# Optimization experiments

Measured on AMD Instinct MI355X. Metric: run time of the kernel, lower is better.

Reference implementation:

```python
import jax, jax.numpy as jnp
import numpy as np

N_NODES = 100000
N_EDGES = 1600000
D_IN = 128
D_OUT = 128
N_GRAPHS = 256


def setup_inputs() -> dict:
    key = jax.random.key(0)
    k1, k2, k3, k4 = jax.random.split(key, 4)
    H = jax.random.normal(k1, (N_NODES, D_IN), dtype=jnp.float32)
    edge_index = jax.random.randint(k2, (2, N_EDGES), 0, N_NODES, dtype=jnp.int64)
    batch = jnp.sort(jax.random.randint(k3, (N_NODES,), 0, N_GRAPHS, dtype=jnp.int64))
    # Kaiming-normal init: std = sqrt(2 / fan_in)
    W = jax.random.normal(k4, (D_IN, D_OUT), dtype=jnp.float32) * np.float32(np.sqrt(2.0 / D_IN))
    return {"H": H, "edge_index": edge_index, "batch": batch, "W": W}


def reference(H, edge_index, batch, W):
    N = H.shape[0]
    src, dst = edge_index[0], edge_index[1]
    # message passing: gather source features, scatter_add into destinations
    agg = jax.ops.segment_sum(H[src], dst, num_segments=N)  # [N, D]
    out = H + agg
    # virtual node: per-graph mean, broadcast back to nodes
    sums = jax.ops.segment_sum(out, batch, num_segments=N_GRAPHS)            # [G, D]
    counts = jax.ops.segment_sum(jnp.ones((N, 1), out.dtype), batch,
                                 num_segments=N_GRAPHS)                       # [G, 1]
    vmean = sums / jnp.maximum(counts, 1.0)
    out = out + vmean[batch]
    # dense transform + activation
    return jax.nn.relu(out @ W)
```

## Files before the change

### kernel.cpp

```cpp
#include <hip/hip_runtime.h>

#define DIM 128
#define NGRAPH 256

#define CHUNK 512
#define CHB 9
#define MAXNB 256
#define EPB 4096
#define EPT (EPB / 256)
#define FCAP 14336

typedef __attribute__((ext_vector_type(8))) short short8;
typedef __attribute__((ext_vector_type(4))) float f32x4;

__device__ inline unsigned int bpack2(float lo, float hi) {
  unsigned int ul = __float_as_uint(lo);
  unsigned int uh = __float_as_uint(hi);
  ul = (ul + 0x7fffu + ((ul >> 16) & 1u)) >> 16;
  uh = (uh + 0x7fffu + ((uh >> 16) & 1u)) & 0xffff0000u;
  return ul | uh;
}

__device__ inline float4 bunpack4(uint2 v) {
  float4 r;
  r.x = __uint_as_float(v.x << 16);
  r.y = __uint_as_float(v.x & 0xffff0000u);
  r.z = __uint_as_float(v.y << 16);
  r.w = __uint_as_float(v.y & 0xffff0000u);
  return r;
}

__global__ __launch_bounds__(256) void k_prep(const float4* __restrict__ H4,
    uint2* __restrict__ Hb, int n4,
    const int* __restrict__ dst, unsigned short* __restrict__ bh, int E,
    int NBLK) {
  __shared__ unsigned int hist[MAXNB];
  int blk = blockIdx.x, t = threadIdx.x;
  int i = blk * 256 + t;
  if (i < n4) {
    float4 a = H4[i];
    uint2 r;
    r.x = bpack2(a.x, a.y);
    r.y = bpack2(a.z, a.w);
    Hb[i] = r;
  }
  if (blk < NBLK) {
    hist[t] = 0;
    __syncthreads();
    int base = blk * EPB;
#pragma unroll
    for (int k = 0; k < EPT; ++k) {
      int e = base + k * 256 + t;
      if (e < E) atomicAdd(&hist[((unsigned)dst[e]) >> CHB], 1);
    }
    __syncthreads();
    bh[(size_t)blk * MAXNB + t] = (unsigned short)hist[t];
  }
}

__global__ __launch_bounds__(256) void k_bhist(const int* __restrict__ dst,
    unsigned short* __restrict__ bh, int E) {
  __shared__ unsigned int hist[MAXNB];
  int blk = blockIdx.x, t = threadIdx.x;
  hist[t] = 0;
  __syncthreads();
  int base = blk * EPB;
#pragma unroll
  for (int i = 0; i < EPT; ++i) {
    int e = base + i * 256 + t;
    if (e < E) atomicAdd(&hist[((unsigned)dst[e]) >> CHB], 1);
  }
  __syncthreads();
  bh[(size_t)blk * MAXNB + t] = (unsigned short)hist[t];
}

__global__ __launch_bounds__(256) void k_bscan(unsigned short* __restrict__ bh,
    unsigned int* __restrict__ btot, int NBLK) {
  __shared__ unsigned int tmp[256];
  int b = blockIdx.x, t = threadIdx.x;
  int i0 = 2 * t, i1 = 2 * t + 1;
  unsigned int a0 = (i0 < NBLK) ? bh[(size_t)i0 * MAXNB + b] : 0u;
  unsigned int a1 = (i1 < NBLK) ? bh[(size_t)i1 * MAXNB + b] : 0u;
  unsigned int ps = a0 + a1;
  tmp[t] = ps;
  __syncthreads();
  for (int off = 1; off < 256; off <<= 1) {
    unsigned int x = (t >= off) ? tmp[t - off] : 0u;
    __syncthreads();
    tmp[t] += x;
    __syncthreads();
  }
  unsigned int ex = tmp[t] - ps;
  if (i0 < NBLK) bh[(size_t)i0 * MAXNB + b] = (unsigned short)ex;
  if (i1 < NBLK) bh[(size_t)i1 * MAXNB + b] = (unsigned short)(ex + a0);
  if (t == 255) btot[b] = tmp[255];
}

__global__ __launch_bounds__(256) void k_bscan2(const unsigned int* __restrict__ btot,
    unsigned int* __restrict__ bbase, int* __restrict__ offs, int N, int E) {
  __shared__ unsigned int s[256];
  int t = threadIdx.x;
  unsigned int v = btot[t];
  s[t] = v;
  __syncthreads();
  for (int off = 1; off < 256; off <<= 1) {
    unsigned int x = (t >= off) ? s[t - off] : 0u;
    __syncthreads();
    s[t] += x;
    __syncthreads();
  }
  bbase[t] = s[t] - v;
  if (t == 255) { bbase[256] = s[255]; offs[N] = E; }
}

__global__ __launch_bounds__(256) void k_part(const int* __restrict__ src,
    const int* __restrict__ dst, const unsigned short* __restrict__ bh,
    const unsigned int* __restrict__ bbase, unsigned int* __restrict__ pack, int E) {
  __shared__ unsigned int hist[MAXNB];
  __shared__ unsigned int sc[MAXNB];
  __shared__ unsigned int gbase[MAXNB];
  __shared__ unsigned int lpack[EPB];
  __shared__ unsigned short lbkt[EPB];
  __shared__ unsigned int totS;
  int blk = blockIdx.x, t = threadIdx.x;
  hist[t] = 0;
  __syncthreads();

  int base = blk * EPB;
  unsigned int pk[EPT];
  int bk[EPT];
  unsigned int rk[EPT];
#pragma unroll
  for (int i = 0; i < EPT; ++i) {
    int e = base + i * 256 + t;
    if (e < E) {
      unsigned int s = (unsigned)src[e], d = (unsigned)dst[e];
      pk[i] = (s << CHB) | (d & (CHUNK - 1));
      int b = (int)(d >> CHB);
      bk[i] = b;
      rk[i] = atomicAdd(&hist[b], 1u);
    } else {
      bk[i] = -1;
    }
  }
  __syncthreads();

  unsigned int c = hist[t];
  sc[t] = c;
  __syncthreads();
  for (int off = 1; off < 256; off <<= 1) {
    unsigned int x = (t >= off) ? sc[t - off] : 0u;
    __syncthreads();
    sc[t] += x;
    __syncthreads();
  }
  if (t == 255) totS = sc[255];
  hist[t] = sc[t] - c;
  gbase[t] = bbase[t] + (unsigned int)bh[(size_t)blk * MAXNB + t];
  __syncthreads();

#pragma unroll
  for (int i = 0; i < EPT; ++i) {
    if (bk[i] >= 0) {
      unsigned int slot = hist[bk[i]] + rk[i];
      lpack[slot] = pk[i];
      lbkt[slot] = (unsigned short)bk[i];
    }
  }
  __syncthreads();

  unsigned int tot = totS;
  for (unsigned int s = t; s < tot; s += 256) {
    int b = lbkt[s];
    unsigned int local = s - hist[b];
    pack[gbase[b] + local] = lpack[s];
  }
}

__global__ __launch_bounds__(256) void k_fine(unsigned int* __restrict__ pack,
    const unsigned int* __restrict__ bbase, int* __restrict__ offs, int N) {
  __shared__ unsigned int lp[FCAP];
  __shared__ unsigned int cnt[CHUNK];
  __shared__ unsigned int cur[CHUNK];
  __shared__ unsigned int tmp[256];
  int b = blockIdx.x, t = threadIdx.x;
  unsigned int lo = bbase[b], hi = bbase[b + 1];
  int n = (int)(hi - lo);
  if (n > FCAP) n = FCAP;
  cnt[2 * t] = 0; cnt[2 * t + 1] = 0;
  __syncthreads();
  for (int i = t; i < n; i += 256) {
    unsigned int p = pack[lo + i];
    lp[i] = p;
    atomicAdd(&cnt[p & (CHUNK - 1)], 1u);
  }
  __syncthreads();
  unsigned int c0 = cnt[2 * t], c1 = cnt[2 * t + 1];
  unsigned int ps = c0 + c1;
  tmp[t] = ps;
  __syncthreads();
  for (int off = 1; off < 256; off <<= 1) {
    unsigned int x = (t >= off) ? tmp[t - off] : 0u;
    __syncthreads();
    tmp[t] += x;
    __syncthreads();
  }
  unsigned int ex = tmp[t] - ps;
  cur[2 * t] = ex;
  cur[2 * t + 1] = ex + c0;
  __syncthreads();
  int nb0 = b * CHUNK;
#pragma unroll
  for (int j = t; j < CHUNK; j += 256) {
    int node = nb0 + j;
    if (node < N) offs[node] = (int)(lo + cur[j]);
  }
  __syncthreads();
  for (int i = t; i < n; i += 256) {
    unsigned int p = lp[i];
    unsigned int r = atomicAdd(&cur[p & (CHUNK - 1)], 1u);
    pack[lo + r] = p;
  }
}

__device__ inline void bacc(uint2 v, float4& a) {
  a.x += __uint_as_float(v.x << 16);
  a.y += __uint_as_float(v.x & 0xffff0000u);
  a.z += __uint_as_float(v.y << 16);
  a.w += __uint_as_float(v.y & 0xffff0000u);
}

__global__ __launch_bounds__(256) void k_gatherbx(const uint2* __restrict__ Hb,
    const int* __restrict__ offs, const unsigned int* __restrict__ pack,
    uint2* __restrict__ Hx, int n) {
  int gid = blockIdx.x * 256 + threadIdx.x;
  int node = gid >> 6;
  if (node >= n) return;
  int lane = threadIdx.x & 63;
  int half = lane >> 5, q = lane & 31;
  float4 A = {0,0,0,0}, B = {0,0,0,0}, C = {0,0,0,0}, D = {0,0,0,0};
  int beg = offs[node], end = offs[node + 1];
  int j = beg + half;
  for (; j + 6 < end; j += 8) {
    uint2 v0 = Hb[(size_t)(pack[j + 0] >> CHB) * 32 + q];
    uint2 v1 = Hb[(size_t)(pack[j + 2] >> CHB) * 32 + q];
    uint2 v2 = Hb[(size_t)(pack[j + 4] >> CHB) * 32 + q];
    uint2 v3 = Hb[(size_t)(pack[j + 6] >> CHB) * 32 + q];
    bacc(v0, A); bacc(v1, B); bacc(v2, C); bacc(v3, D);
  }
  for (; j < end; j += 2) bacc(Hb[(size_t)(pack[j] >> CHB) * 32 + q], A);
  A.x += B.x + (C.x + D.x);
  A.y += B.y + (C.y + D.y);
  A.z += B.z + (C.z + D.z);
  A.w += B.w + (C.w + D.w);
  A.x += __shfl_xor(A.x, 32);
  A.y += __shfl_xor(A.y, 32);
  A.z += __shfl_xor(A.z, 32);
  A.w += __shfl_xor(A.w, 32);
  if (half == 0) {
    float4 b4 = bunpack4(Hb[(size_t)node * 32 + q]);
    uint2 o;
    o.x = bpack2(b4.x + A.x, b4.y + A.y);
    o.y = bpack2(b4.z + A.z, b4.w + A.w);
    Hx[(size_t)node * 32 + q] = o;
  }
}

__global__ __launch_bounds__(256) void k_gatherb(const float* __restrict__ H,
    const uint2* __restrict__ Hb, const int* __restrict__ offs,
    const unsigned int* __restrict__ pack, float* __restrict__ out, int n) {
  int gid = blockIdx.x * 256 + threadIdx.x;
  int node = gid >> 6;
  if (node >= n) return;
  int lane = threadIdx.x & 63;
  int half = lane >> 5, q = lane & 31;
  float4 A = {0,0,0,0}, B = {0,0,0,0}, C = {0,0,0,0}, D = {0,0,0,0};
  int beg = offs[node], end = offs[node + 1];
  int j = beg + half;
  for (; j + 6 < end; j += 8) {
    uint2 v0 = Hb[(size_t)(pack[j + 0] >> CHB) * 32 + q];
    uint2 v1 = Hb[(size_t)(pack[j + 2] >> CHB) * 32 + q];
    uint2 v2 = Hb[(size_t)(pack[j + 4] >> CHB) * 32 + q];
    uint2 v3 = Hb[(size_t)(pack[j + 6] >> CHB) * 32 + q];
    bacc(v0, A); bacc(v1, B); bacc(v2, C); bacc(v3, D);
  }
  for (; j < end; j += 2) bacc(Hb[(size_t)(pack[j] >> CHB) * 32 + q], A);
  A.x += B.x + (C.x + D.x);
  A.y += B.y + (C.y + D.y);
  A.z += B.z + (C.z + D.z);
  A.w += B.w + (C.w + D.w);
  A.x += __shfl_xor(A.x, 32);
  A.y += __shfl_xor(A.y, 32);
  A.z += __shfl_xor(A.z, 32);
  A.w += __shfl_xor(A.w, 32);
  if (half == 0) {
    float4 b4 = ((const float4*)H)[(size_t)node * 32 + q];
    float4 r;
    r.x = b4.x + A.x; r.y = b4.y + A.y; r.z = b4.z + A.z; r.w = b4.w + A.w;
    ((float4*)out)[(size_t)node * 32 + q] = r;
  }
}

__global__ __launch_bounds__(256) void k_gather(const float* __restrict__ H,
    const int* __restrict__ offs, const unsigned int* __restrict__ pack,
    float* __restrict__ out, int n) {
  int gid = blockIdx.x * 256 + threadIdx.x;
  int node = gid >> 6;
  if (node >= n) return;
  int lane = threadIdx.x & 63;
  const float2* H2 = (const float2*)H;
  float2 base = H2[(size_t)node * 64 + lane];
  float2 s0 = {0.f, 0.f}, s1 = {0.f, 0.f};
  int beg = offs[node], end = offs[node + 1];
  int j = beg;
  for (; j + 2 <= end; j += 2) {
    float2 v0 = H2[(size_t)(pack[j + 0] >> CHB) * 64 + lane];
    float2 v1 = H2[(size_t)(pack[j + 1] >> CHB) * 64 + lane];
    s0.x += v0.x; s0.y += v0.y;
    s1.x += v1.x; s1.y += v1.y;
  }
  for (; j < end; ++j) {
    float2 v = H2[(size_t)(pack[j] >> CHB) * 64 + lane];
    s0.x += v.x; s0.y += v.y;
  }
  float2 r;
  r.x = base.x + s0.x + s1.x;
  r.y = base.y + s0.y + s1.y;
  ((float2*)out)[(size_t)node * 64 + lane] = r;
}

__global__ __launch_bounds__(256) void k_init(const float4* __restrict__ s,
                                              float4* __restrict__ d, int n4) {
  int i = blockIdx.x * 256 + threadIdx.x;
  if (i < n4) d[i] = s[i];
}

__global__ __launch_bounds__(256) void k_scatter(const float* __restrict__ H,
    const int* __restrict__ src, const int* __restrict__ dst,
    float* __restrict__ out, int nE) {
  long long idx = (long long)blockIdx.x * 256 + threadIdx.x;
  int e = (int)(idx >> 5);
  if (e >= nE) return;
  int q = (int)(idx & 31);
  int s = src[e];
  int t = dst[e];
  const float4 h = *(const float4*)(H + (size_t)s * DIM + q * 4);
  float* o = out + (size_t)t * DIM + q * 4;
  unsafeAtomicAdd(o + 0, h.x);
  unsafeAtomicAdd(o + 1, h.y);
  unsafeAtomicAdd(o + 2, h.z);
  unsafeAtomicAdd(o + 3, h.w);
}

__global__ __launch_bounds__(256) void k_vmean4x(const uint2* __restrict__ hx,
    const int* __restrict__ batch, float* __restrict__ vmean, int n) {
  int g = blockIdx.x >> 2, c = blockIdx.x & 3;
  int lo = 0, hi = n;
  while (lo < hi) { int m = (lo + hi) >> 1; if (batch[m] < g) lo = m + 1; else hi = m; }
  int start = lo;
  hi = n;
  while (lo < hi) { int m = (lo + hi) >> 1; if (batch[m] < g + 1) lo = m + 1; else hi = m; }
  int end = lo;

  int t = threadIdx.x, rg = t >> 3, s = t & 7;
  int d4 = c * 8 + s;
  float4 acc = {0,0,0,0};
  for (int r = start + rg; r < end; r += 32) {
    float4 v = bunpack4(hx[(size_t)r * 32 + d4]);
    acc.x += v.x; acc.y += v.y; acc.z += v.z; acc.w += v.w;
  }
  __shared__ float4 sd[256];
  sd[t] = acc;
  __syncthreads();
  for (int off = 16; off >= 1; off >>= 1) {
    if (rg < off) {
      float4 o = sd[t + off * 8];
      acc.x += o.x; acc.y += o.y; acc.z += o.z; acc.w += o.w;
      sd[t] = acc;
    }
    __syncthreads();
  }
  if (rg == 0) {
    float cnt = fmaxf((float)(end - start), 1.0f);
    float4 r;
    r.x = acc.x / cnt; r.y = acc.y / cnt; r.z = acc.z / cnt; r.w = acc.w / cnt;
    ((float4*)vmean)[g * 32 + d4] = r;
  }
}

__global__ __launch_bounds__(256) void k_vmean4(const float* __restrict__ x,
    const int* __restrict__ batch, float* __restrict__ vmean, int n) {
  int g = blockIdx.x >> 2, c = blockIdx.x & 3;
  int lo = 0, hi = n;
  while (lo < hi) { int m = (lo + hi) >> 1; if (batch[m] < g) lo = m + 1; else hi = m; }
  int start = lo;
  hi = n;
  while (lo < hi) { int m = (lo + hi) >> 1; if (batch[m] < g + 1) lo = m + 1; else hi = m; }
  int end = lo;

  int t = threadIdx.x, rg = t >> 3, s = t & 7;
  int d4 = c * 8 + s;
  const float4* x4 = (const float4*)x;
  float4 acc = {0,0,0,0};
  for (int r = start + rg; r < end; r += 32) {
    float4 v = x4[(size_t)r * 32 + d4];
    acc.x += v.x; acc.y += v.y; acc.z += v.z; acc.w += v.w;
  }
  __shared__ float4 sd[256];
  sd[t] = acc;
  __syncthreads();
  for (int off = 16; off >= 1; off >>= 1) {
    if (rg < off) {
      float4 o = sd[t + off * 8];
      acc.x += o.x; acc.y += o.y; acc.z += o.z; acc.w += o.w;
      sd[t] = acc;
    }
    __syncthreads();
  }
  if (rg == 0) {
    float cnt = fmaxf((float)(end - start), 1.0f);
    float4 r;
    r.x = acc.x / cnt; r.y = acc.y / cnt; r.z = acc.z / cnt; r.w = acc.w / cnt;
    ((float4*)vmean)[g * 32 + d4] = r;
  }
}

__global__ __launch_bounds__(256) void k_wprep(const float* __restrict__ W,
                                               uint4* __restrict__ wt) {
  int gid = blockIdx.x * 256 + threadIdx.x;
  int col = gid >> 4, chunk = gid & 15;
  float f[8];
#pragma unroll
  for (int j = 0; j < 8; ++j) f[j] = W[(chunk * 8 + j) * DIM + col];
  uint4 u;
  u.x = bpack2(f[0], f[1]);
  u.y = bpack2(f[2], f[3]);
  u.z = bpack2(f[4], f[5]);
  u.w = bpack2(f[6], f[7]);
  wt[col * 16 + (chunk ^ (col & 7))] = u;
}

__global__ __launch_bounds__(256) void k_mfmax(const uint4* __restrict__ Hx,
    float* __restrict__ io, const int* __restrict__ batch,
    const float* __restrict__ vmean, const uint4* __restrict__ wt, int n) {
  __shared__ uint4 WtL[2048];
  int tid = threadIdx.x;
#pragma unroll
  for (int j = 0; j < 8; ++j) WtL[tid + 256 * j] = wt[tid + 256 * j];
  __syncthreads();

  int wid = tid >> 6;
  int lane = tid & 63;
  int q = lane & 15, hi = lane >> 4;
  int row0 = blockIdx.x * 128 + wid * 32;

  f32x4 acc[2][8];
#pragma unroll
  for (int m = 0; m < 2; ++m)
#pragma unroll
    for (int nn = 0; nn < 8; ++nn) acc[m][nn] = (f32x4){0.f, 0.f, 0.f, 0.f};

  bool okm[2];
  const uint4* xrow[2];
  const float4* vrow[2];
#pragma unroll
  for (int m = 0; m < 2; ++m) {
    int row = row0 + m * 16 + q;
    bool ok = row < n;
    okm[m] = ok;
    int g = ok ? batch[row] : 0;
    xrow[m] = Hx + (size_t)row * 16;
    vrow[m] = (const float4*)vmean + (size_t)g * 32;
  }

  for (int kk = 0; kk < 4; ++kk) {
    short8 Bf[8];
#pragma unroll
    for (int nn = 0; nn < 8; ++nn) {
      int colrow = nn * 16 + q;
      int idx = colrow * 16 + ((kk * 4 + hi) ^ (colrow & 7));
      Bf[nn] = *(short8*)&WtL[idx];
    }
    short8 Af[2];
#pragma unroll
    for (int m = 0; m < 2; ++m) {
      uint4 u = {0, 0, 0, 0};
      if (okm[m]) {
        uint4 xv = xrow[m][kk * 4 + hi];
        float4 x0 = bunpack4(*(uint2*)&xv.x);
        float4 x1 = bunpack4(*(uint2*)&xv.z);
        int c = kk * 8 + hi * 2;
        float4 v0 = vrow[m][c], v1 = vrow[m][c + 1];
        u.x = bpack2(x0.x + v0.x, x0.y + v0.y);
        u.y = bpack2(x0.z + v0.z, x0.w + v0.w);
        u.z = bpack2(x1.x + v1.x, x1.y + v1.y);
        u.w = bpack2(x1.z + v1.z, x1.w + v1.w);
      }
      Af[m] = *(short8*)&u;
    }
#pragma unroll
    for (int nn = 0; nn < 8; ++nn) {
      acc[0][nn] = __builtin_amdgcn_mfma_f32_16x16x32_bf16(Af[0], Bf[nn], acc[0][nn], 0, 0, 0);
      acc[1][nn] = __builtin_amdgcn_mfma_f32_16x16x32_bf16(Af[1], Bf[nn], acc[1][nn], 0, 0, 0);
    }
  }

#pragma unroll
  for (int m = 0; m < 2; ++m) {
    int grow0 = row0 + m * 16 + hi * 4;
#pragma unroll
    for (int nn = 0; nn < 8; ++nn) {
      int gcol = nn * 16 + q;
      f32x4 c = acc[m][nn];
#pragma unroll
      for (int r = 0; r < 4; ++r) {
        int grow = grow0 + r;
        if (grow < n) io[(size_t)grow * DIM + gcol] = fmaxf(c[r], 0.f);
      }
    }
  }
}

__global__ __launch_bounds__(256) void k_mfma(float* __restrict__ io,
    const int* __restrict__ batch, const float* __restrict__ vmean,
    const uint4* __restrict__ wt, int n) {
  __shared__ uint4 WtL[2048];
  int tid = threadIdx.x;
#pragma unroll
  for (int j = 0; j < 8; ++j) WtL[tid + 256 * j] = wt[tid + 256 * j];
  __syncthreads();

  int wid = tid >> 6;
  int lane = tid & 63;
  int q = lane & 15, hi = lane >> 4;
  int row0 = blockIdx.x * 128 + wid * 32;

  f32x4 acc[2][8];
#pragma unroll
  for (int m = 0; m < 2; ++m)
#pragma unroll
    for (int nn = 0; nn < 8; ++nn) acc[m][nn] = (f32x4){0.f, 0.f, 0.f, 0.f};

  bool okm[2];
  const float4* xrow[2];
  const float4* vrow[2];
#pragma unroll
  for (int m = 0; m < 2; ++m) {
    int row = row0 + m * 16 + q;
    bool ok = row < n;
    okm[m] = ok;
    int g = ok ? batch[row] : 0;
    xrow[m] = (const float4*)io + (size_t)row * 32;
    vrow[m] = (const float4*)vmean + (size_t)g * 32;
  }

  for (int kk = 0; kk < 4; ++kk) {
    short8 Bf[8];
#pragma unroll
    for (int nn = 0; nn < 8; ++nn) {
      int colrow = nn * 16 + q;
      int idx = colrow * 16 + ((kk * 4 + hi) ^ (colrow & 7));
      Bf[nn] = *(short8*)&WtL[idx];
    }
    short8 Af[2];
#pragma unroll
    for (int m = 0; m < 2; ++m) {
      float4 x0 = {0,0,0,0}, x1 = {0,0,0,0};
      if (okm[m]) {
        int c = kk * 8 + hi * 2;
        float4 a0 = xrow[m][c], a1 = xrow[m][c + 1];
        float4 v0 = vrow[m][c], v1 = vrow[m][c + 1];
        x0.x = a0.x + v0.x; x0.y = a0.y + v0.y; x0.z = a0.z + v0.z; x0.w = a0.w + v0.w;
        x1.x = a1.x + v1.x; x1.y = a1.y + v1.y; x1.z = a1.z + v1.z; x1.w = a1.w + v1.w;
      }
      uint4 u;
      u.x = bpack2(x0.x, x0.y);
      u.y = bpack2(x0.z, x0.w);
      u.z = bpack2(x1.x, x1.y);
      u.w = bpack2(x1.z, x1.w);
      Af[m] = *(short8*)&u;
    }
#pragma unroll
    for (int nn = 0; nn < 8; ++nn) {
      acc[0][nn] = __builtin_amdgcn_mfma_f32_16x16x32_bf16(Af[0], Bf[nn], acc[0][nn], 0, 0, 0);
      acc[1][nn] = __builtin_amdgcn_mfma_f32_16x16x32_bf16(Af[1], Bf[nn], acc[1][nn], 0, 0, 0);
    }
  }

#pragma unroll
  for (int m = 0; m < 2; ++m) {
    int grow0 = row0 + m * 16 + hi * 4;
#pragma unroll
    for (int nn = 0; nn < 8; ++nn) {
      int gcol = nn * 16 + q;
      f32x4 c = acc[m][nn];
#pragma unroll
      for (int r = 0; r < 4; ++r) {
        int grow = grow0 + r;
        if (grow < n) io[(size_t)grow * DIM + gcol] = fmaxf(c[r], 0.f);
      }
    }
  }
}

#define TRR 64
__global__ __launch_bounds__(256) void k_gemm(float* __restrict__ io,
    const int* __restrict__ batch, const float* __restrict__ vmean,
    const float* __restrict__ W, int n) {
  __shared__ float xs[TRR][DIM + 1];
  __shared__ float Wl[DIM][64];
  int tid = threadIdx.x;
  int row0 = blockIdx.x * TRR;

  for (int i = tid; i < TRR * 32; i += 256) {
    int r = i >> 5, c4 = i & 31;
    int row = row0 + r;
    float4 a;
    if (row < n) {
      int g = batch[row];
      float4 xv = *((const float4*)(io + (size_t)row * DIM) + c4);
      float4 vv = *((const float4*)(vmean + (size_t)g * DIM) + c4);
      a.x = xv.x + vv.x; a.y = xv.y + vv.y; a.z = xv.z + vv.z; a.w = xv.w + vv.w;
    } else {
      a.x = a.y = a.z = a.w = 0.f;
    }
    xs[r][c4 * 4 + 0] = a.x;
    xs[r][c4 * 4 + 1] = a.y;
    xs[r][c4 * 4 + 2] = a.z;
    xs[r][c4 * 4 + 3] = a.w;
  }

  int cg = tid & 15;
  int rg = tid >> 4;
  float acc[4][4];

  for (int jh = 0; jh < 2; ++jh) {
    __syncthreads();
    for (int i = tid; i < DIM * 16; i += 256) {
      int k = i >> 4, c4 = i & 15;
      *(float4*)&Wl[k][c4 * 4] =
          *(const float4*)(W + (size_t)k * DIM + jh * 64 + c4 * 4);
    }
    __syncthreads();

#pragma unroll
    for (int a = 0; a < 4; ++a)
#pragma unroll
      for (int b = 0; b < 4; ++b) acc[a][b] = 0.f;

    for (int k = 0; k < DIM; ++k) {
      float4 wv = *(const float4*)&Wl[k][cg * 4];
#pragma unroll
      for (int a = 0; a < 4; ++a) {
        float xv = xs[rg * 4 + a][k];
        acc[a][0] += xv * wv.x;
        acc[a][1] += xv * wv.y;
        acc[a][2] += xv * wv.z;
        acc[a][3] += xv * wv.w;
      }
    }

#pragma unroll
    for (int a = 0; a < 4; ++a) {
      int row = row0 + rg * 4 + a;
      if (row < n) {
        float4 o;
        o.x = fmaxf(acc[a][0], 0.f);
        o.y = fmaxf(acc[a][1], 0.f);
        o.z = fmaxf(acc[a][2], 0.f);
        o.w = fmaxf(acc[a][3], 0.f);
        *(float4*)(io + (size_t)row * DIM + jh * 64 + cg * 4) = o;
      }
    }
  }
}

extern "C" void kernel_launch(void* const* d_in, const int* in_sizes, int n_in,
                              void* d_out, int out_size, void* d_ws, size_t ws_size,
                              hipStream_t stream) {
  const float* H     = (const float*)d_in[0];
  const int*   ei    = (const int*)d_in[1];
  const int*   batch = (const int*)d_in[2];
  const float* W     = (const float*)d_in[3];
  float* out = (float*)d_out;

  int N = in_sizes[0] / DIM;
  int E = in_sizes[1] / 2;
  const int* src = ei;
  const int* dst = ei + E;

  int NB   = (N + CHUNK - 1) >> CHB;
  int NBLK = (E + EPB - 1) / EPB;

  size_t o = 0;
  auto carve = [&](size_t bytes) -> void* {
    void* p = (char*)d_ws + o;
    o = (o + bytes + 255) & ~(size_t)255;
    return p;
  };
  unsigned int*   pack  = (unsigned int*)carve((size_t)E * 4);
  int*            offs  = (int*)carve(((size_t)N + 1) * 4);
  unsigned short* bh    = (unsigned short*)carve((size_t)NBLK * MAXNB * 2);
  unsigned int*   btot  = (unsigned int*)carve(MAXNB * 4);
  unsigned int*   bbase = (unsigned int*)carve((MAXNB + 1) * 4);
  size_t o_csr = o;
  uint2*          Hb    = (uint2*)carve((size_t)N * DIM * 2);
  size_t o_bf = o;
  uint4*          wt    = (uint4*)carve((size_t)DIM * DIM * 2);
  size_t o_wt = o;
  uint2*          Hx    = (uint2*)carve((size_t)N * DIM * 2);
  size_t o_hx = o;
  float* vmean = (float*)bh;

  bool csr_ok = (o_csr <= ws_size) && (NB >= 1) && (NB <= MAXNB) &&
                (NBLK <= 512) && ((size_t)NBLK * MAXNB * 2 >= (size_t)NGRAPH * DIM * 4) &&
                (E / NB <= 8192);
  bool bf_ok = csr_ok && (o_bf <= ws_size);
  bool wt_ok = bf_ok && (o_wt <= ws_size) && (DIM == 128);
  bool hx_ok = wt_ok && (o_hx <= ws_size);

  if (csr_ok) {
    if (bf_ok) {
      int n4 = N * DIM / 4;
      int gprep = (n4 + 255) / 256;
      if (gprep < NBLK) gprep = NBLK;
      k_prep<<<gprep, 256, 0, stream>>>((const float4*)H, Hb, n4, dst, bh, E, NBLK);
    } else {
      k_bhist<<<NBLK, 256, 0, stream>>>(dst, bh, E);
    }
    k_bscan<<<MAXNB, 256, 0, stream>>>(bh, btot, NBLK);
    k_bscan2<<<1, 256, 0, stream>>>(btot, bbase, offs, N, E);
    k_part<<<NBLK, 256, 0, stream>>>(src, dst, bh, bbase, pack, E);
    k_fine<<<NB, 256, 0, stream>>>(pack, bbase, offs, N);
    long long gthreads = (long long)N * 64;
    int gblocks = (int)((gthreads + 255) / 256);
    if (hx_ok) {
      k_gatherbx<<<gblocks, 256, 0, stream>>>(Hb, offs, pack, Hx, N);
      k_vmean4x<<<NGRAPH * 4, 256, 0, stream>>>(Hx, batch, vmean, N);
      k_wprep<<<8, 256, 0, stream>>>(W, wt);
      k_mfmax<<<(N + 127) / 128, 256, 0, stream>>>((const uint4*)Hx, out, batch, vmean, wt, N);
      return;
    }
    if (bf_ok) {
      k_gatherb<<<gblocks, 256, 0, stream>>>(H, Hb, offs, pack, out, N);
    } else {
      k_gather<<<gblocks, 256, 0, stream>>>(H, offs, pack, out, N);
    }
  } else {
    vmean = (float*)d_ws;
    int n4 = N * DIM / 4;
    k_init<<<(n4 + 255) / 256, 256, 0, stream>>>((const float4*)H, (float4*)out, n4);
    long long sthreads = (long long)E * 32;
    k_scatter<<<(int)((sthreads + 255) / 256), 256, 0, stream>>>(H, src, dst, out, E);
  }

  k_vmean4<<<NGRAPH * 4, 256, 0, stream>>>(out, batch, vmean, N);

  if (wt_ok) {
    k_wprep<<<8, 256, 0, stream>>>(W, wt);
    k_mfma<<<(N + 127) / 128, 256, 0, stream>>>(out, batch, vmean, wt, N);
  } else {
    k_gemm<<<(N + TRR - 1) / TRR, 256, 0, stream>>>(out, batch, vmean, W, N);
  }
}
```

Before: 159.2 us.

## Widen gather to 16-byte loads, fold W prep into prep kernel, add nontemporal hints

The gather kernel now has each lane load 16 bytes (8 bf16 values), with four 16-lane groups per wavefront each taking every fourth edge, and the group results are reduced with two shuffle stages. The W bf16 packing moves into k_prep, which removes one kernel launch. Nontemporal loads and stores are added on H, pack, Hx and the final output to limit cache pollution. The wider loads halve the number of gather requests, at the cost of more accumulator registers and an extra shuffle reduction stage.

Result: slower. 170.3 us (+7.0%).

```diff
diff --git a/kernel.cpp b/kernel.cpp
--- a/kernel.cpp
+++ b/kernel.cpp
@@ -12,6 +12,7 @@
 
 typedef __attribute__((ext_vector_type(8))) short short8;
 typedef __attribute__((ext_vector_type(4))) float f32x4;
+typedef __attribute__((ext_vector_type(4))) unsigned int u32x4;
 
 __device__ inline unsigned int bpack2(float lo, float hi) {
   unsigned int ul = __float_as_uint(lo);
@@ -30,19 +31,32 @@
   return r;
 }
 
-__global__ __launch_bounds__(256) void k_prep(const float4* __restrict__ H4,
+__global__ __launch_bounds__(256) void k_prep(const float* __restrict__ Hf,
     uint2* __restrict__ Hb, int n4,
     const int* __restrict__ dst, unsigned short* __restrict__ bh, int E,
-    int NBLK) {
+    int NBLK, const float* __restrict__ W, uint4* __restrict__ wt, int dowt) {
   __shared__ unsigned int hist[MAXNB];
   int blk = blockIdx.x, t = threadIdx.x;
   int i = blk * 256 + t;
   if (i < n4) {
-    float4 a = H4[i];
+    f32x4 a = __builtin_nontemporal_load((const f32x4*)Hf + i);
     uint2 r;
     r.x = bpack2(a.x, a.y);
     r.y = bpack2(a.z, a.w);
     Hb[i] = r;
+  }
+  if (dowt && blk < 8) {
+    int gid = blk * 256 + t;
+    int col = gid >> 4, chunk = gid & 15;
+    float f[8];
+#pragma unroll
+    for (int j = 0; j < 8; ++j) f[j] = W[(chunk * 8 + j) * DIM + col];
+    uint4 u;
+    u.x = bpack2(f[0], f[1]);
+    u.y = bpack2(f[2], f[3]);
+    u.z = bpack2(f[4], f[5]);
+    u.w = bpack2(f[6], f[7]);
+    wt[col * 16 + (chunk ^ (col & 7))] = u;
   }
   if (blk < NBLK) {
     hist[t] = 0;
@@ -223,47 +237,76 @@
   }
 }
 
+__device__ inline void bacc4(uint4 v, float4& lo, float4& hi) {
+  lo.x += __uint_as_float(v.x << 16);
+  lo.y += __uint_as_float(v.x & 0xffff0000u);
+  lo.z += __uint_as_float(v.y << 16);
+  lo.w += __uint_as_float(v.y & 0xffff0000u);
+  hi.x += __uint_as_float(v.z << 16);
+  hi.y += __uint_as_float(v.z & 0xffff0000u);
+  hi.z += __uint_as_float(v.w << 16);
+  hi.w += __uint_as_float(v.w & 0xffff0000u);
+}
+
+__global__ __launch_bounds__(256) void k_gather4x(const uint4* __restrict__ Hb4,
+    const int* __restrict__ offs, const unsigned int* __restrict__ pack,
+    unsigned int* __restrict__ Hx, int n) {
+  int gid = blockIdx.x * 256 + threadIdx.x;
+  int node = gid >> 6;
+  if (node >= n) return;
+  int lane = threadIdx.x & 63;
+  int grp = lane >> 4, q = lane & 15;
+  float4 a0 = {0,0,0,0}, a1 = {0,0,0,0};
+  float4 b0 = {0,0,0,0}, b1 = {0,0,0,0};
+  float4 c0 = {0,0,0,0}, c1 = {0,0,0,0};
+  float4 d0 = {0,0,0,0}, d1 = {0,0,0,0};
+  int beg = offs[node], end = offs[node + 1];
+  int j = beg + grp;
+  for (; j + 12 < end; j += 16) {
+    unsigned int p0 = __builtin_nontemporal_load(&pack[j + 0]);
+    unsigned int p1 = __builtin_nontemporal_load(&pack[j + 4]);
+    unsigned int p2 = __builtin_nontemporal_load(&pack[j + 8]);
+    unsigned int p3 = __builtin_nontemporal_load(&pack[j + 12]);
+    uint4 v0 = Hb4[(size_t)(p0 >> CHB) * 16 + q];
+    uint4 v1 = Hb4[(size_t)(p1 >> CHB) * 16 + q];
+    uint4 v2 = Hb4[(size_t)(p2 >> CHB) * 16 + q];
+    uint4 v3 = Hb4[(size_t)(p3 >> CHB) * 16 + q];
+    bacc4(v0, a0, a1); bacc4(v1, b0, b1); bacc4(v2, c0, c1); bacc4(v3, d0, d1);
+  }
+  for (; j < end; j += 4) {
+    unsigned int p = __builtin_nontemporal_load(&pack[j]);
+    bacc4(Hb4[(size_t)(p >> CHB) * 16 + q], a0, a1);
+  }
+  a0.x += b0.x + (c0.x + d0.x);  a1.x += b1.x + (c1.x + d1.x);
+  a0.y += b0.y + (c0.y + d0.y);  a1.y += b1.y + (c1.y + d1.y);
+  a0.z += b0.z + (c0.z + d0.z);  a1.z += b1.z + (c1.z + d1.z);
+  a0.w += b0.w + (c0.w + d0.w);  a1.w += b1.w + (c1.w + d1.w);
+  a0.x += __shfl_xor(a0.x, 16);  a1.x += __shfl_xor(a1.x, 16);
+  a0.y += __shfl_xor(a0.y, 16);  a1.y += __shfl_xor(a1.y, 16);
+  a0.z += __shfl_xor(a0.z, 16);  a1.z += __shfl_xor(a1.z, 16);
+  a0.w += __shfl_xor(a0.w, 16);  a1.w += __shfl_xor(a1.w, 16);
+  a0.x += __shfl_xor(a0.x, 32);  a1.x += __shfl_xor(a1.x, 32);
+  a0.y += __shfl_xor(a0.y, 32);  a1.y += __shfl_xor(a1.y, 32);
+  a0.z += __shfl_xor(a0.z, 32);  a1.z += __shfl_xor(a1.z, 32);
+  a0.w += __shfl_xor(a0.w, 32);  a1.w += __shfl_xor(a1.w, 32);
+  if (grp == 0) {
+    uint4 bs = Hb4[(size_t)node * 16 + q];
+    float4 e0 = {0,0,0,0}, e1 = {0,0,0,0};
+    bacc4(bs, e0, e1);
+    u32x4 o;
+    o.x = bpack2(e0.x + a0.x, e0.y + a0.y);
+    o.y = bpack2(e0.z + a0.z, e0.w + a0.w);
+    o.z = bpack2(e1.x + a1.x, e1.y + a1.y);
+    o.w = bpack2(e1.z + a1.z, e1.w + a1.w);
+    __builtin_nontemporal_store(o, (u32x4*)Hx + (size_t)node * 16 + q);
+  }
+}
+
 __device__ inline void bacc(uint2 v, float4& a) {
   a.x += __uint_as_float(v.x << 16);
   a.y += __uint_as_float(v.x & 0xffff0000u);
   a.z += __uint_as_float(v.y << 16);
   a.w += __uint_as_float(v.y & 0xffff0000u);
-}
-
-__global__ __launch_bounds__(256) void k_gatherbx(const uint2* __restrict__ Hb,
-    const int* __restrict__ offs, const unsigned int* __restrict__ pack,
-    uint2* __restrict__ Hx, int n) {
-  int gid = blockIdx.x * 256 + threadIdx.x;
-  int node = gid >> 6;
-  if (node >= n) return;
-  int lane = threadIdx.x & 63;
-  int half = lane >> 5, q = lane & 31;
-  float4 A = {0,0,0,0}, B = {0,0,0,0}, C = {0,0,0,0}, D = {0,0,0,0};
-  int beg = offs[node], end = offs[node + 1];
-  int j = beg + half;
-  for (; j + 6 < end; j += 8) {
-    uint2 v0 = Hb[(size_t)(pack[j + 0] >> CHB) * 32 + q];
-    uint2 v1 = Hb[(size_t)(pack[j + 2] >> CHB) * 32 + q];
-    uint2 v2 = Hb[(size_t)(pack[j + 4] >> CHB) * 32 + q];
-    uint2 v3 = Hb[(size_t)(pack[j + 6] >> CHB) * 32 + q];
-    bacc(v0, A); bacc(v1, B); bacc(v2, C); bacc(v3, D);
-  }
-  for (; j < end; j += 2) bacc(Hb[(size_t)(pack[j] >> CHB) * 32 + q], A);
-  A.x += B.x + (C.x + D.x);
-  A.y += B.y + (C.y + D.y);
-  A.z += B.z + (C.z + D.z);
-  A.w += B.w + (C.w + D.w);
-  A.x += __shfl_xor(A.x, 32);
-  A.y += __shfl_xor(A.y, 32);
-  A.z += __shfl_xor(A.z, 32);
-  A.w += __shfl_xor(A.w, 32);
-  if (half == 0) {
-    float4 b4 = bunpack4(Hb[(size_t)node * 32 + q]);
-    uint2 o;
-    o.x = bpack2(b4.x + A.x, b4.y + A.y);
-    o.y = bpack2(b4.z + A.z, b4.w + A.w);
-    Hx[(size_t)node * 32 + q] = o;
-  }
 }
 
 __global__ __launch_bounds__(256) void k_gatherb(const float* __restrict__ H,
@@ -515,7 +558,8 @@
 #pragma unroll
       for (int r = 0; r < 4; ++r) {
         int grow = grow0 + r;
-        if (grow < n) io[(size_t)grow * DIM + gcol] = fmaxf(c[r], 0.f);
+        if (grow < n)
+          __builtin_nontemporal_store(fmaxf(c[r], 0.f), &io[(size_t)grow * DIM + gcol]);
       }
     }
   }
@@ -724,7 +768,8 @@
       int n4 = N * DIM / 4;
       int gprep = (n4 + 255) / 256;
       if (gprep < NBLK) gprep = NBLK;
-      k_prep<<<gprep, 256, 0, stream>>>((const float4*)H, Hb, n4, dst, bh, E, NBLK);
+      k_prep<<<gprep, 256, 0, stream>>>(H, Hb, n4, dst, bh, E, NBLK,
+                                        W, wt, hx_ok ? 1 : 0);
     } else {
       k_bhist<<<NBLK, 256, 0, stream>>>(dst, bh, E);
     }
@@ -735,9 +780,9 @@
     long long gthreads = (long long)N * 64;
     int gblocks = (int)((gthreads + 255) / 256);
     if (hx_ok) {
-      k_gatherbx<<<gblocks, 256, 0, stream>>>(Hb, offs, pack, Hx, N);
+      k_gather4x<<<gblocks, 256, 0, stream>>>((const uint4*)Hb, offs, pack,
+                                              (unsigned int*)Hx, N);
       k_vmean4x<<<NGRAPH * 4, 256, 0, stream>>>(Hx, batch, vmean, N);
-      k_wprep<<<8, 256, 0, stream>>>(W, wt);
       k_mfmax<<<(N + 127) / 128, 256, 0, stream>>>((const uint4*)Hx, out, batch, vmean, wt, N);
       return;
     }
```

## Precompute vmean@W per graph, fold small kernels into neighbors, add nontemporal IO

Applied to the files above, without the earlier changes.

Uses linearity, (x+v)W = xW + vW, to compute a per-graph VW table in a tiny kernel, so the MFMA kernel multiplies the raw aggregated rows and adds VW[batch] in the epilogue instead of unpacking, adding and repacking per element. The single-block bscan2 kernel is removed by recomputing the 256-entry scan redundantly inside k_part and k_fine, and W preparation moves into k_prep, cutting launches. Nontemporal loads and stores are used for the streaming H read and the output write. The main risk is a small numeric change, since the mean is no longer rounded to bf16 together with x, plus some redundant scan work in every block.

Result: slower. 172.5 us (+8.4%).

```diff
diff --git a/kernel.cpp b/kernel.cpp
--- a/kernel.cpp
+++ b/kernel.cpp
@@ -30,19 +30,32 @@
   return r;
 }
 
-__global__ __launch_bounds__(256) void k_prep(const float4* __restrict__ H4,
+__global__ __launch_bounds__(256) void k_prep(const float* __restrict__ Hf,
     uint2* __restrict__ Hb, int n4,
     const int* __restrict__ dst, unsigned short* __restrict__ bh, int E,
-    int NBLK) {
+    int NBLK, const float* __restrict__ W, uint4* __restrict__ wt, int dowt) {
   __shared__ unsigned int hist[MAXNB];
   int blk = blockIdx.x, t = threadIdx.x;
   int i = blk * 256 + t;
   if (i < n4) {
-    float4 a = H4[i];
+    f32x4 a = __builtin_nontemporal_load((const f32x4*)Hf + i);
     uint2 r;
     r.x = bpack2(a.x, a.y);
     r.y = bpack2(a.z, a.w);
     Hb[i] = r;
+  }
+  if (dowt && blk < 8) {
+    int gid = blk * 256 + t;
+    int col = gid >> 4, chunk = gid & 15;
+    float f[8];
+#pragma unroll
+    for (int j = 0; j < 8; ++j) f[j] = W[(chunk * 8 + j) * DIM + col];
+    uint4 u;
+    u.x = bpack2(f[0], f[1]);
+    u.y = bpack2(f[2], f[3]);
+    u.z = bpack2(f[4], f[5]);
+    u.w = bpack2(f[6], f[7]);
+    wt[col * 16 + (chunk ^ (col & 7))] = u;
   }
   if (blk < NBLK) {
     hist[t] = 0;
@@ -96,26 +109,9 @@
   if (t == 255) btot[b] = tmp[255];
 }
 
-__global__ __launch_bounds__(256) void k_bscan2(const unsigned int* __restrict__ btot,
-    unsigned int* __restrict__ bbase, int* __restrict__ offs, int N, int E) {
-  __shared__ unsigned int s[256];
-  int t = threadIdx.x;
-  unsigned int v = btot[t];
-  s[t] = v;
-  __syncthreads();
-  for (int off = 1; off < 256; off <<= 1) {
-    unsigned int x = (t >= off) ? s[t - off] : 0u;
-    __syncthreads();
-    s[t] += x;
-    __syncthreads();
-  }
-  bbase[t] = s[t] - v;
-  if (t == 255) { bbase[256] = s[255]; offs[N] = E; }
-}
-
 __global__ __launch_bounds__(256) void k_part(const int* __restrict__ src,
     const int* __restrict__ dst, const unsigned short* __restrict__ bh,
-    const unsigned int* __restrict__ bbase, unsigned int* __restrict__ pack, int E) {
+    const unsigned int* __restrict__ btot, unsigned int* __restrict__ pack, int E) {
   __shared__ unsigned int hist[MAXNB];
   __shared__ unsigned int sc[MAXNB];
   __shared__ unsigned int gbase[MAXNB];
@@ -123,7 +119,18 @@
   __shared__ unsigned short lbkt[EPB];
   __shared__ unsigned int totS;
   int blk = blockIdx.x, t = threadIdx.x;
+
   hist[t] = 0;
+  unsigned int bt = btot[t];
+  sc[t] = bt;
+  __syncthreads();
+  for (int off = 1; off < 256; off <<= 1) {
+    unsigned int x = (t >= off) ? sc[t - off] : 0u;
+    __syncthreads();
+    sc[t] += x;
+    __syncthreads();
+  }
+  gbase[t] = sc[t] - bt;
   __syncthreads();
 
   int base = blk * EPB;
@@ -156,7 +163,7 @@
   }
   if (t == 255) totS = sc[255];
   hist[t] = sc[t] - c;
-  gbase[t] = bbase[t] + (unsigned int)bh[(size_t)blk * MAXNB + t];
+  gbase[t] += (unsigned int)bh[(size_t)blk * MAXNB + t];
   __syncthreads();
 
 #pragma unroll
@@ -178,13 +185,28 @@
 }
 
 __global__ __launch_bounds__(256) void k_fine(unsigned int* __restrict__ pack,
-    const unsigned int* __restrict__ bbase, int* __restrict__ offs, int N) {
+    const unsigned int* __restrict__ btot, int* __restrict__ offs, int N, int E) {
   __shared__ unsigned int lp[FCAP];
   __shared__ unsigned int cnt[CHUNK];
   __shared__ unsigned int cur[CHUNK];
   __shared__ unsigned int tmp[256];
+  __shared__ unsigned int loS, hiS;
   int b = blockIdx.x, t = threadIdx.x;
-  unsigned int lo = bbase[b], hi = bbase[b + 1];
+
+  unsigned int bt = btot[t];
+  tmp[t] = bt;
+  __syncthreads();
+  for (int off = 1; off < 256; off <<= 1) {
+    unsigned int x = (t >= off) ? tmp[t - off] : 0u;
+    __syncthreads();
+    tmp[t] += x;
+    __syncthreads();
+  }
+  if (t == b) { loS = tmp[t] - bt; hiS = tmp[t]; }
+  if (b == 0 && t == 0) offs[N] = E;
+  __syncthreads();
+  unsigned int lo = loS, hi = hiS;
+
   int n = (int)(hi - lo);
   if (n > FCAP) n = FCAP;
   cnt[2 * t] = 0; cnt[2 * t + 1] = 0;
@@ -425,6 +447,16 @@
   }
 }
 
+__global__ __launch_bounds__(128) void k_vw(const float* __restrict__ vmean,
+    const float* __restrict__ W, float* __restrict__ VW) {
+  int g = blockIdx.x, col = threadIdx.x;
+  const float* vr = vmean + (size_t)g * DIM;
+  float acc = 0.f;
+#pragma unroll 8
+  for (int k = 0; k < DIM; ++k) acc += vr[k] * W[(size_t)k * DIM + col];
+  VW[(size_t)g * DIM + col] = acc;
+}
+
 __global__ __launch_bounds__(256) void k_wprep(const float* __restrict__ W,
                                                uint4* __restrict__ wt) {
   int gid = blockIdx.x * 256 + threadIdx.x;
@@ -442,7 +474,7 @@
 
 __global__ __launch_bounds__(256) void k_mfmax(const uint4* __restrict__ Hx,
     float* __restrict__ io, const int* __restrict__ batch,
-    const float* __restrict__ vmean, const uint4* __restrict__ wt, int n) {
+    const float* __restrict__ VW, const uint4* __restrict__ wt, int n) {
   __shared__ uint4 WtL[2048];
   int tid = threadIdx.x;
 #pragma unroll
@@ -462,15 +494,11 @@
 
   bool okm[2];
   const uint4* xrow[2];
-  const float4* vrow[2];
 #pragma unroll
   for (int m = 0; m < 2; ++m) {
     int row = row0 + m * 16 + q;
-    bool ok = row < n;
-    okm[m] = ok;
-    int g = ok ? batch[row] : 0;
+    okm[m] = row < n;
     xrow[m] = Hx + (size_t)row * 16;
-    vrow[m] = (const float4*)vmean + (size_t)g * 32;
   }
 
   for (int kk = 0; kk < 4; ++kk) {
@@ -485,17 +513,7 @@
 #pragma unroll
     for (int m = 0; m < 2; ++m) {
       uint4 u = {0, 0, 0, 0};
-      if (okm[m]) {
-        uint4 xv = xrow[m][kk * 4 + hi];
-        float4 x0 = bunpack4(*(uint2*)&xv.x);
-        float4 x1 = bunpack4(*(uint2*)&xv.z);
-        int c = kk * 8 + hi * 2;
-        float4 v0 = vrow[m][c], v1 = vrow[m][c + 1];
-        u.x = bpack2(x0.x + v0.x, x0.y + v0.y);
-        u.y = bpack2(x0.z + v0.z, x0.w + v0.w);
-        u.z = bpack2(x1.x + v1.x, x1.y + v1.y);
-        u.w = bpack2(x1.z + v1.z, x1.w + v1.w);
-      }
+      if (okm[m]) u = xrow[m][kk * 4 + hi];
       Af[m] = *(short8*)&u;
     }
 #pragma unroll
@@ -508,6 +526,12 @@
 #pragma unroll
   for (int m = 0; m < 2; ++m) {
     int grow0 = row0 + m * 16 + hi * 4;
+    int gg[4];
+#pragma unroll
+    for (int r = 0; r < 4; ++r) {
+      int grow = grow0 + r;
+      gg[r] = (grow < n) ? batch[grow] : 0;
+    }
 #pragma unroll
     for (int nn = 0; nn < 8; ++nn) {
       int gcol = nn * 16 + q;
@@ -515,7 +539,11 @@
 #pragma unroll
       for (int r = 0; r < 4; ++r) {
         int grow = grow0 + r;
-        if (grow < n) io[(size_t)grow * DIM + gcol] = fmaxf(c[r], 0.f);
+        if (grow < n) {
+          float v = VW[(size_t)gg[r] * DIM + gcol];
+          __builtin_nontemporal_store(fmaxf(c[r] + v, 0.f),
+                                      &io[(size_t)grow * DIM + gcol]);
+        }
       }
     }
   }
@@ -702,12 +730,12 @@
   int*            offs  = (int*)carve(((size_t)N + 1) * 4);
   unsigned short* bh    = (unsigned short*)carve((size_t)NBLK * MAXNB * 2);
   unsigned int*   btot  = (unsigned int*)carve(MAXNB * 4);
-  unsigned int*   bbase = (unsigned int*)carve((MAXNB + 1) * 4);
   size_t o_csr = o;
   uint2*          Hb    = (uint2*)carve((size_t)N * DIM * 2);
   size_t o_bf = o;
   uint4*          wt    = (uint4*)carve((size_t)DIM * DIM * 2);
   size_t o_wt = o;
+  float*          VW    = (float*)carve((size_t)NGRAPH * DIM * 4);
   uint2*          Hx    = (uint2*)carve((size_t)N * DIM * 2);
   size_t o_hx = o;
   float* vmean = (float*)bh;
@@ -724,21 +752,21 @@
       int n4 = N * DIM / 4;
       int gprep = (n4 + 255) / 256;
       if (gprep < NBLK) gprep = NBLK;
-      k_prep<<<gprep, 256, 0, stream>>>((const float4*)H, Hb, n4, dst, bh, E, NBLK);
+      k_prep<<<gprep, 256, 0, stream>>>(H, Hb, n4, dst, bh, E, NBLK,
+                                        W, wt, hx_ok ? 1 : 0);
     } else {
       k_bhist<<<NBLK, 256, 0, stream>>>(dst, bh, E);
     }
     k_bscan<<<MAXNB, 256, 0, stream>>>(bh, btot, NBLK);
-    k_bscan2<<<1, 256, 0, stream>>>(btot, bbase, offs, N, E);
-    k_part<<<NBLK, 256, 0, stream>>>(src, dst, bh, bbase, pack, E);
-    k_fine<<<NB, 256, 0, stream>>>(pack, bbase, offs, N);
+    k_part<<<NBLK, 256, 0, stream>>>(src, dst, bh, btot, pack, E);
+    k_fine<<<NB, 256, 0, stream>>>(pack, btot, offs, N, E);
     long long gthreads = (long long)N * 64;
     int gblocks = (int)((gthreads + 255) / 256);
     if (hx_ok) {
       k_gatherbx<<<gblocks, 256, 0, stream>>>(Hb, offs, pack, Hx, N);
       k_vmean4x<<<NGRAPH * 4, 256, 0, stream>>>(Hx, batch, vmean, N);
-      k_wprep<<<8, 256, 0, stream>>>(W, wt);
-      k_mfmax<<<(N + 127) / 128, 256, 0, stream>>>((const uint4*)Hx, out, batch, vmean, wt, N);
+      k_vw<<<NGRAPH, 128, 0, stream>>>(vmean, W, VW);
+      k_mfmax<<<(N + 127) / 128, 256, 0, stream>>>((const uint4*)Hx, out, batch, VW, wt, N);
       return;
     }
     if (bf_ok) {
```

## Move H bf16 conversion into partition kernel and fold W prep into histogram

Applied to the files above, without the earlier changes.

The H-to-bf16 conversion moves from the histogram kernel into the partition kernel, and the histogram kernel now also does the W transpose/pack, which removes the separate k_wprep launch. The histogram pass becomes lightweight and the conversion overlaps with the partition work, cutting one launch. The final ReLU output store and the H load now use nontemporal hints. The risk is that the partition kernel's grid grows to cover the conversion, which may add contention.

Result: no change. 162.0 us (+1.8%).

```diff
diff --git a/kernel.cpp b/kernel.cpp
--- a/kernel.cpp
+++ b/kernel.cpp
@@ -30,48 +30,36 @@
   return r;
 }
 
-__global__ __launch_bounds__(256) void k_prep(const float4* __restrict__ H4,
-    uint2* __restrict__ Hb, int n4,
-    const int* __restrict__ dst, unsigned short* __restrict__ bh, int E,
-    int NBLK) {
+__global__ __launch_bounds__(256) void k_bhistw(const int* __restrict__ dst,
+    unsigned short* __restrict__ bh, int E, int NBLK,
+    const float* __restrict__ W, uint4* __restrict__ wt, int dowt) {
   __shared__ unsigned int hist[MAXNB];
   int blk = blockIdx.x, t = threadIdx.x;
-  int i = blk * 256 + t;
-  if (i < n4) {
-    float4 a = H4[i];
-    uint2 r;
-    r.x = bpack2(a.x, a.y);
-    r.y = bpack2(a.z, a.w);
-    Hb[i] = r;
+  if (dowt && blk < 8) {
+    int gid = blk * 256 + t;
+    int col = gid >> 4, chunk = gid & 15;
+    float f[8];
+#pragma unroll
+    for (int j = 0; j < 8; ++j) f[j] = W[(chunk * 8 + j) * DIM + col];
+    uint4 u;
+    u.x = bpack2(f[0], f[1]);
+    u.y = bpack2(f[2], f[3]);
+    u.z = bpack2(f[4], f[5]);
+    u.w = bpack2(f[6], f[7]);
+    wt[col * 16 + (chunk ^ (col & 7))] = u;
   }
   if (blk < NBLK) {
     hist[t] = 0;
     __syncthreads();
     int base = blk * EPB;
 #pragma unroll
-    for (int k = 0; k < EPT; ++k) {
-      int e = base + k * 256 + t;
+    for (int i = 0; i < EPT; ++i) {
+      int e = base + i * 256 + t;
       if (e < E) atomicAdd(&hist[((unsigned)dst[e]) >> CHB], 1);
     }
     __syncthreads();
     bh[(size_t)blk * MAXNB + t] = (unsigned short)hist[t];
   }
-}
-
-__global__ __launch_bounds__(256) void k_bhist(const int* __restrict__ dst,
-    unsigned short* __restrict__ bh, int E) {
-  __shared__ unsigned int hist[MAXNB];
-  int blk = blockIdx.x, t = threadIdx.x;
-  hist[t] = 0;
-  __syncthreads();
-  int base = blk * EPB;
-#pragma unroll
-  for (int i = 0; i < EPT; ++i) {
-    int e = base + i * 256 + t;
-    if (e < E) atomicAdd(&hist[((unsigned)dst[e]) >> CHB], 1);
-  }
-  __syncthreads();
-  bh[(size_t)blk * MAXNB + t] = (unsigned short)hist[t];
 }
 
 __global__ __launch_bounds__(256) void k_bscan(unsigned short* __restrict__ bh,
@@ -113,9 +101,10 @@
   if (t == 255) { bbase[256] = s[255]; offs[N] = E; }
 }
 
-__global__ __launch_bounds__(256) void k_part(const int* __restrict__ src,
+__global__ __launch_bounds__(256) void k_partc(const int* __restrict__ src,
     const int* __restrict__ dst, const unsigned short* __restrict__ bh,
-    const unsigned int* __restrict__ bbase, unsigned int* __restrict__ pack, int E) {
+    const unsigned int* __restrict__ bbase, unsigned int* __restrict__ pack, int E,
+    const float* __restrict__ Hf, uint2* __restrict__ Hb, int n4c) {
   __shared__ unsigned int hist[MAXNB];
   __shared__ unsigned int sc[MAXNB];
   __shared__ unsigned int gbase[MAXNB];
@@ -123,57 +112,70 @@
   __shared__ unsigned short lbkt[EPB];
   __shared__ unsigned int totS;
   int blk = blockIdx.x, t = threadIdx.x;
-  hist[t] = 0;
-  __syncthreads();
-
-  int base = blk * EPB;
-  unsigned int pk[EPT];
-  int bk[EPT];
-  unsigned int rk[EPT];
-#pragma unroll
-  for (int i = 0; i < EPT; ++i) {
-    int e = base + i * 256 + t;
-    if (e < E) {
-      unsigned int s = (unsigned)src[e], d = (unsigned)dst[e];
-      pk[i] = (s << CHB) | (d & (CHUNK - 1));
-      int b = (int)(d >> CHB);
-      bk[i] = b;
-      rk[i] = atomicAdd(&hist[b], 1u);
-    } else {
-      bk[i] = -1;
-    }
-  }
-  __syncthreads();
-
-  unsigned int c = hist[t];
-  sc[t] = c;
-  __syncthreads();
-  for (int off = 1; off < 256; off <<= 1) {
-    unsigned int x = (t >= off) ? sc[t - off] : 0u;
-    __syncthreads();
-    sc[t] += x;
-    __syncthreads();
-  }
-  if (t == 255) totS = sc[255];
-  hist[t] = sc[t] - c;
-  gbase[t] = bbase[t] + (unsigned int)bh[(size_t)blk * MAXNB + t];
-  __syncthreads();
-
-#pragma unroll
-  for (int i = 0; i < EPT; ++i) {
-    if (bk[i] >= 0) {
-      unsigned int slot = hist[bk[i]] + rk[i];
-      lpack[slot] = pk[i];
-      lbkt[slot] = (unsigned short)bk[i];
-    }
-  }
-  __syncthreads();
-
-  unsigned int tot = totS;
-  for (unsigned int s = t; s < tot; s += 256) {
-    int b = lbkt[s];
-    unsigned int local = s - hist[b];
-    pack[gbase[b] + local] = lpack[s];
+
+  int ci = blk * 256 + t;
+  if (ci < n4c) {
+    f32x4 a = __builtin_nontemporal_load((const f32x4*)Hf + ci);
+    uint2 r;
+    r.x = bpack2(a.x, a.y);
+    r.y = bpack2(a.z, a.w);
+    Hb[ci] = r;
+  }
+  if (blk >= gridDim.x) return;
+
+  if (blk < ((E + EPB - 1) / EPB)) {
+    hist[t] = 0;
+    __syncthreads();
+
+    int base = blk * EPB;
+    unsigned int pk[EPT];
+    int bk[EPT];
+    unsigned int rk[EPT];
+#pragma unroll
+    for (int i = 0; i < EPT; ++i) {
+      int e = base + i * 256 + t;
+      if (e < E) {
+        unsigned int s = (unsigned)src[e], d = (unsigned)dst[e];
+        pk[i] = (s << CHB) | (d & (CHUNK - 1));
+        int b = (int)(d >> CHB);
+        bk[i] = b;
+        rk[i] = atomicAdd(&hist[b], 1u);
+      } else {
+        bk[i] = -1;
+      }
+    }
+    __syncthreads();
+
+    unsigned int c = hist[t];
+    sc[t] = c;
+    __syncthreads();
+    for (int off = 1; off < 256; off <<= 1) {
+      unsigned int x = (t >= off) ? sc[t - off] : 0u;
+      __syncthreads();
+      sc[t] += x;
+      __syncthreads();
+    }
+    if (t == 255) totS = sc[255];
+    hist[t] = sc[t] - c;
+    gbase[t] = bbase[t] + (unsigned int)bh[(size_t)blk * MAXNB + t];
+    __syncthreads();
+
+#pragma unroll
+    for (int i = 0; i < EPT; ++i) {
+      if (bk[i] >= 0) {
+        unsigned int slot = hist[bk[i]] + rk[i];
+        lpack[slot] = pk[i];
+        lbkt[slot] = (unsigned short)bk[i];
+      }
+    }
+    __syncthreads();
+
+    unsigned int tot = totS;
+    for (unsigned int s = t; s < tot; s += 256) {
+      int b = lbkt[s];
+      unsigned int local = s - hist[b];
+      pack[gbase[b] + local] = lpack[s];
+    }
   }
 }
 
@@ -329,6 +331,22 @@
   ((float2*)out)[(size_t)node * 64 + lane] = r;
 }
 
+__global__ __launch_bounds__(256) void k_bhist(const int* __restrict__ dst,
+    unsigned short* __restrict__ bh, int E) {
+  __shared__ unsigned int hist[MAXNB];
+  int blk = blockIdx.x, t = threadIdx.x;
+  hist[t] = 0;
+  __syncthreads();
+  int base = blk * EPB;
+#pragma unroll
+  for (int i = 0; i < EPT; ++i) {
+    int e = base + i * 256 + t;
+    if (e < E) atomicAdd(&hist[((unsigned)dst[e]) >> CHB], 1);
+  }
+  __syncthreads();
+  bh[(size_t)blk * MAXNB + t] = (unsigned short)hist[t];
+}
+
 __global__ __launch_bounds__(256) void k_init(const float4* __restrict__ s,
                                               float4* __restrict__ d, int n4) {
   int i = blockIdx.x * 256 + threadIdx.x;
@@ -515,7 +533,8 @@
 #pragma unroll
       for (int r = 0; r < 4; ++r) {
         int grow = grow0 + r;
-        if (grow < n) io[(size_t)grow * DIM + gcol] = fmaxf(c[r], 0.f);
+        if (grow < n)
+          __builtin_nontemporal_store(fmaxf(c[r], 0.f), &io[(size_t)grow * DIM + gcol]);
       }
     }
   }
@@ -720,24 +739,22 @@
   bool hx_ok = wt_ok && (o_hx <= ws_size);
 
   if (csr_ok) {
-    if (bf_ok) {
-      int n4 = N * DIM / 4;
-      int gprep = (n4 + 255) / 256;
-      if (gprep < NBLK) gprep = NBLK;
-      k_prep<<<gprep, 256, 0, stream>>>((const float4*)H, Hb, n4, dst, bh, E, NBLK);
-    } else {
-      k_bhist<<<NBLK, 256, 0, stream>>>(dst, bh, E);
-    }
+    int n4 = N * DIM / 4;
+    int hgrid = NBLK;
+    if (hx_ok && hgrid < 8) hgrid = 8;
+    k_bhistw<<<hgrid, 256, 0, stream>>>(dst, bh, E, NBLK, W, wt, hx_ok ? 1 : 0);
     k_bscan<<<MAXNB, 256, 0, stream>>>(bh, btot, NBLK);
     k_bscan2<<<1, 256, 0, stream>>>(btot, bbase, offs, N, E);
-    k_part<<<NBLK, 256, 0, stream>>>(src, dst, bh, bbase, pack, E);
+    int n4c = bf_ok ? n4 : 0;
+    int pgrid = NBLK;
+    if (bf_ok) { int cg = (n4 + 255) / 256; if (cg > pgrid) pgrid = cg; }
+    k_partc<<<pgrid, 256, 0, stream>>>(src, dst, bh, bbase, pack, E, H, Hb, n4c);
     k_fine<<<NB, 256, 0, stream>>>(pack, bbase, offs, N);
     long long gthreads = (long long)N * 64;
     int gblocks = (int)((gthreads + 255) / 256);
     if (hx_ok) {
       k_gatherbx<<<gblocks, 256, 0, stream>>>(Hb, offs, pack, Hx, N);
       k_vmean4x<<<NGRAPH * 4, 256, 0, stream>>>(Hx, batch, vmean, N);
-      k_wprep<<<8, 256, 0, stream>>>(W, wt);
       k_mfmax<<<(N + 127) / 128, 256, 0, stream>>>((const uint4*)Hx, out, batch, vmean, wt, N);
       return;
     }
```
